# Kernel tuning notes

Measured on AMD Instinct MI355X. Metric: run time of the kernel, lower is better.

## Reference

```python
import jax, jax.numpy as jnp
import numpy as np

D_MODEL = 1024
N_HEADS = 16
HEAD_DIM = D_MODEL // N_HEADS  # 64


def setup_inputs() -> dict:
    key = jax.random.key(0)
    k1, k2, k3 = jax.random.split(key, 3)
    B, T = 2, 2048
    x = jax.random.normal(k1, (B, T, D_MODEL), dtype=jnp.float32)
    # nn.Linear(d, 3d) weight applied as x @ W (stored transposed vs torch)
    W_qkv = jax.random.normal(k2, (D_MODEL, 3 * D_MODEL), dtype=jnp.float32) / np.sqrt(D_MODEL)
    W_proj = jax.random.normal(k3, (D_MODEL, D_MODEL), dtype=jnp.float32) / np.sqrt(D_MODEL)
    return {"x": x, "W_qkv": W_qkv, "W_proj": W_proj}


def reference(x, W_qkv, W_proj):
    B, T, D = x.shape
    qkv = x @ W_qkv  # [B, T, 3D]
    qkv = qkv.reshape(B, T, 3, N_HEADS, HEAD_DIM)
    qkv = jnp.transpose(qkv, (2, 0, 3, 1, 4))  # [3, B, H, T, hd]
    q, k, v = qkv[0], qkv[1], qkv[2]
    # muP 'readout' attn_score: scale by 1/head_dim (instead of 1/sqrt(head_dim))
    attn = jnp.einsum('bhqd,bhkd->bhqk', q, k) / HEAD_DIM  # [B, H, T, T]
    attn = jax.nn.softmax(attn, axis=-1)
    out = jnp.einsum('bhqk,bhkd->bhqd', attn, v)  # [B, H, T, hd]
    out = jnp.transpose(out, (0, 2, 1, 3)).reshape(B, T, D)
    return out @ W_proj
```

## Files before the change

kernel.cpp:

```cpp
#include <hip/hip_runtime.h>
#include <hip/hip_bf16.h>
#include <hip/hip_fp16.h>
#include <stdint.h>

#define B_    2
#define T_    2048
#define DM    1024
#define NH    16
#define HD    64
#define M_    (B_ * T_)
#define N_QKV (3 * DM)

typedef __attribute__((ext_vector_type(8))) __bf16 bf16x8;
typedef __attribute__((ext_vector_type(4))) float  v4f;
typedef __attribute__((ext_vector_type(4))) _Float16 h4;
typedef __attribute__((ext_vector_type(8))) _Float16 h8;
typedef __hip_bfloat16 bf16;

__device__ __forceinline__ void gld_lds16(const void* g, void* l) {
  __builtin_amdgcn_global_load_lds(
      (const __attribute__((address_space(1))) void*)(g),
      (__attribute__((address_space(3))) void*)(l), 16, 0, 0);
}


__global__ void cast_f32_bf16(const float* __restrict__ in, bf16* __restrict__ out) {
  int i = (blockIdx.x * 256 + threadIdx.x) * 4;
  float4 v = *(const float4*)(in + i);
  union { bf16 h[4]; ushort4 u; } r;
  r.h[0] = __float2bfloat16(v.x); r.h[1] = __float2bfloat16(v.y);
  r.h[2] = __float2bfloat16(v.z); r.h[3] = __float2bfloat16(v.w);
  *(ushort4*)(out + i) = r.u;
}

__global__ void transpose_cast(const float* __restrict__ in, bf16* __restrict__ out,
                               int R, int C) {
  __shared__ float tile[32][33];
  int c0 = blockIdx.x * 32, r0 = blockIdx.y * 32;
  int tx = threadIdx.x, ty = threadIdx.y;
  #pragma unroll
  for (int i = ty; i < 32; i += 8)
    tile[i][tx] = in[(size_t)(r0 + i) * C + c0 + tx];
  __syncthreads();
  #pragma unroll
  for (int i = ty; i < 32; i += 8)
    out[(size_t)(c0 + i) * R + r0 + tx] = __float2bfloat16(tile[tx][i]);
}

__global__ __launch_bounds__(256) void transpose_v(
    const _Float16* __restrict__ in, _Float16* __restrict__ out) {
  __shared__ _Float16 tl[64][72];
  const int tid = threadIdx.x, bh = blockIdx.y, t0 = blockIdx.x * 64;
  const size_t ib = (size_t)bh * T_ * HD, ob = (size_t)bh * HD * T_;
  #pragma unroll
  for (int i = 0; i < 2; ++i) {
    int flat = (i * 256 + tid) * 8;
    int r = flat >> 6, c = flat & 63;
    *(uint4*)(&tl[r][c]) = *(const uint4*)(in + ib + (size_t)(t0 + r) * HD + c);
  }
  __syncthreads();
  int d = tid >> 2, c0 = (tid & 3) * 16;
  #pragma unroll
  for (int j = 0; j < 16; j += 8) {
    union { _Float16 h[8]; uint4 u; } pk;
    #pragma unroll
    for (int k2 = 0; k2 < 8; ++k2) pk.h[k2] = tl[c0 + j + k2][d];
    *(uint4*)(out + ob + (size_t)d * T_ + t0 + c0 + j) = pk.u;
  }
}

template <int MODE>
__global__ __launch_bounds__(256) void gemm_bt(
    const bf16* __restrict__ A, const bf16* __restrict__ BT,
    float* __restrict__ Cf, bf16* __restrict__ qb, bf16* __restrict__ kb,
    _Float16* __restrict__ vb, int M, int N, int K) {
  __shared__ bf16 As[128 * 64];
  __shared__ bf16 Bs[128 * 64];
  const int tid = threadIdx.x;
  const int l = tid & 63, w = tid >> 6;
  const int wm = w >> 1, wn = w & 1;
  const int m0 = blockIdx.y * 128, n0 = blockIdx.x * 128;
  const int fr = l & 15;
  const int lg = l >> 4;

  v4f acc[4][4] = {};

  for (int kt = 0; kt < K; kt += 64) {
    __syncthreads();
    #pragma unroll
    for (int i = 0; i < 4; ++i) {
      int p = i * 256 + tid;
      int row = p >> 3, g = (p & 7) ^ (row & 7);
      gld_lds16(A + (size_t)(m0 + row) * K + kt + g * 8, As + p * 8);
      gld_lds16(BT + (size_t)(n0 + row) * K + kt + g * 8, Bs + p * 8);
    }
    __syncthreads();
    #pragma unroll
    for (int kk = 0; kk < 64; kk += 32) {
      const int gl = (kk >> 3) + lg;
      bf16x8 af[4], bfr[4];
      #pragma unroll
      for (int i = 0; i < 4; ++i) {
        int row = wm * 64 + i * 16 + fr;
        af[i] = *(const bf16x8*)(As + row * 64 + (gl ^ (fr & 7)) * 8);
      }
      #pragma unroll
      for (int i = 0; i < 4; ++i) {
        int row = wn * 64 + i * 16 + fr;
        bfr[i] = *(const bf16x8*)(Bs + row * 64 + (gl ^ (fr & 7)) * 8);
      }
      #pragma unroll
      for (int mi = 0; mi < 4; ++mi)
        #pragma unroll
        for (int ni = 0; ni < 4; ++ni)
          acc[mi][ni] = __builtin_amdgcn_mfma_f32_16x16x32_bf16(
              af[mi], bfr[ni], acc[mi][ni], 0, 0, 0);
    }
  }

  #pragma unroll
  for (int mi = 0; mi < 4; ++mi) {
    #pragma unroll
    for (int ni = 0; ni < 4; ++ni) {
      #pragma unroll
      for (int r = 0; r < 4; ++r) {
        int gm = m0 + wm * 64 + mi * 16 + (l >> 4) * 4 + r;
        int gn = n0 + wn * 64 + ni * 16 + (l & 15);
        float v = acc[mi][ni][r];
        if constexpr (MODE == 0) {
          Cf[(size_t)gm * N + gn] = v;
        } else {
          int b = gm >> 11, t = gm & 2047;
          int s = gn >> 10, h = (gn >> 6) & 15, d = gn & 63;
          size_t bh = (size_t)(b * NH + h);
          if (s == 0)      qb[(bh * T_ + t) * HD + d] = __float2bfloat16(v);
          else if (s == 1) kb[(bh * T_ + t) * HD + d] = __float2bfloat16(v);
          else             vb[(bh * T_ + t) * HD + d] = (_Float16)v;
        }
      }
    }
  }
}

__global__ __launch_bounds__(128) void flash_attn(
    const bf16* __restrict__ Qg, const bf16* __restrict__ Kg,
    const _Float16* __restrict__ VTg, bf16* __restrict__ Og) {
  __shared__ bf16     Ks[128 * 64];
  __shared__ _Float16 Vs[64 * 128];
  __shared__ _Float16 Ps[128][40];
  const int tid = threadIdx.x, l = tid & 63, w = tid >> 6;
  const int bh = blockIdx.y, qt = blockIdx.x;
  const int fr = l & 15, fk = (l >> 4) * 8, g4 = (l >> 4) * 4, lg = l >> 4;
  const int q0 = qt * 128 + w * 64;
  const size_t base  = (size_t)bh * T_ * HD;
  const size_t baseV = (size_t)bh * HD * T_;

  bf16x8 qB[4][2];
  #pragma unroll
  for (int qf = 0; qf < 4; ++qf)
    #pragma unroll
    for (int kki = 0; kki < 2; ++kki)
      qB[qf][kki] = *(const bf16x8*)(
          Qg + base + (size_t)(q0 + qf * 16 + fr) * HD + kki * 32 + fk);

  h8 ones;
  #pragma unroll
  for (int j = 0; j < 8; ++j) ones[j] = (_Float16)1.0f;

  v4f o[4][4] = {};
  v4f lacc[4] = {};

  for (int kt = 0; kt < T_; kt += 128) {
    __syncthreads();
    #pragma unroll
    for (int i = 0; i < 8; ++i) {
      int p = i * 128 + tid;
      int krow = p >> 3, kg = (p & 7) ^ (krow & 7);
      gld_lds16(Kg + base + (size_t)(kt + krow) * HD + kg * 8, Ks + p * 8);
      int vrow = p >> 4, vg = (p & 15) ^ (vrow & 15);
      gld_lds16(VTg + baseV + (size_t)vrow * T_ + kt + vg * 8, Vs + p * 8);
    }
    __syncthreads();

    #pragma unroll
    for (int kk = 0; kk < 4; ++kk) {
      #pragma unroll
      for (int half = 0; half < 2; ++half) {
        const int kf = kk * 2 + half;
        v4f st[4] = {};
        #pragma unroll
        for (int kki = 0; kki < 2; ++kki) {
          int row = kf * 16 + fr;
          bf16x8 ak = *(const bf16x8*)(
              Ks + row * 64 + ((kki * 4 + lg) ^ (fr & 7)) * 8);
          #pragma unroll
          for (int qf = 0; qf < 4; ++qf)
            st[qf] = __builtin_amdgcn_mfma_f32_16x16x32_bf16(
                ak, qB[qf][kki], st[qf], 0, 0, 0);
        }
        #pragma unroll
        for (int qf = 0; qf < 4; ++qf) {
          h4 pv;
          #pragma unroll
          for (int r = 0; r < 4; ++r)
            pv[r] = (_Float16)__expf(st[qf][r] * 0.015625f);
          *(h4*)(&Ps[w * 64 + qf * 16 + fr][half * 16 + g4]) = pv;
        }
      }
      h8 ap[4], bv[4];
      #pragma unroll
      for (int qf = 0; qf < 4; ++qf)
        ap[qf] = *(const h8*)(&Ps[w * 64 + qf * 16 + fr][fk]);
      #pragma unroll
      for (int nf = 0; nf < 4; ++nf) {
        int row = nf * 16 + fr;
        bv[nf] = *(const h8*)(Vs + row * 128 + ((kk * 4 + lg) ^ fr) * 8);
      }
      #pragma unroll
      for (int qf = 0; qf < 4; ++qf) {
        lacc[qf] = __builtin_amdgcn_mfma_f32_16x16x32_f16(
            ap[qf], ones, lacc[qf], 0, 0, 0);
        #pragma unroll
        for (int nf = 0; nf < 4; ++nf)
          o[qf][nf] = __builtin_amdgcn_mfma_f32_16x16x32_f16(
              ap[qf], bv[nf], o[qf][nf], 0, 0, 0);
      }
    }
  }

  int b = bh >> 4, h = bh & 15;
  #pragma unroll
  for (int qf = 0; qf < 4; ++qf) {
    #pragma unroll
    for (int r = 0; r < 4; ++r) {
      float inv = 1.f / lacc[qf][r];
      int t = q0 + qf * 16 + g4 + r;
      #pragma unroll
      for (int nf = 0; nf < 4; ++nf) {
        int d = nf * 16 + fr;
        Og[((size_t)(b * T_ + t)) * DM + h * HD + d] =
            __float2bfloat16(o[qf][nf][r] * inv);
      }
    }
  }
}

extern "C" void kernel_launch(void* const* d_in, const int* in_sizes, int n_in,
                              void* d_out, int out_size, void* d_ws, size_t ws_size,
                              hipStream_t stream) {
  const float* x     = (const float*)d_in[0];
  const float* Wqkv  = (const float*)d_in[1];
  const float* Wproj = (const float*)d_in[2];
  float* out = (float*)d_out;
  char* ws = (char*)d_ws;

  bf16*     Xb     = (bf16*)(ws);
  bf16*     WqkvT  = (bf16*)(ws + (size_t)( 8u << 20));
  bf16*     WprojT = (bf16*)(ws + (size_t)(14u << 20));
  bf16*     Qb     = (bf16*)(ws + (size_t)(16u << 20));
  bf16*     Kb     = (bf16*)(ws + (size_t)(24u << 20));
  _Float16* VTh    = (_Float16*)(ws + (size_t)(32u << 20));
  _Float16* Vh     = (_Float16*)(ws + (size_t)(40u << 20));
  bf16*     Ab     = (bf16*)(ws + (size_t)(40u << 20));

  cast_f32_bf16<<<(M_ * DM) / 1024, 256, 0, stream>>>(x, Xb);
  transpose_cast<<<dim3(N_QKV / 32, DM / 32), dim3(32, 8), 0, stream>>>(Wqkv, WqkvT, DM, N_QKV);
  transpose_cast<<<dim3(DM / 32, DM / 32), dim3(32, 8), 0, stream>>>(Wproj, WprojT, DM, DM);

  gemm_bt<1><<<dim3(N_QKV / 128, M_ / 128), 256, 0, stream>>>(
      Xb, WqkvT, nullptr, Qb, Kb, Vh, M_, N_QKV, DM);

  transpose_v<<<dim3(T_ / 64, B_ * NH), 256, 0, stream>>>(Vh, VTh);

  flash_attn<<<dim3(T_ / 128, B_ * NH), 128, 0, stream>>>(Qb, Kb, VTh, Ab);

  gemm_bt<0><<<dim3(DM / 128, M_ / 128), 256, 0, stream>>>(
      Ab, WprojT, out, nullptr, nullptr, nullptr, M_, DM, DM);
}
```

Before: 215.1 us.

## Split attention keys across warps and split-K the output projection GEMM

Flash attention now runs 256 threads per block: two warp pairs each process half of every 128-key tile, and their partial O and row sums are reduced through shared memory before the write. The softmax exp is rewritten as a raw exp2 with a folded scale and packed fp16 conversion. The output projection GEMM is split along K into two halves that atomically accumulate into a zeroed output, doubling the block count. Costs are an extra memset, atomic traffic, a shared-memory reduction step, and nondeterministic float summation order.

```diff
diff --git a/kernel.cpp b/kernel.cpp
--- a/kernel.cpp
+++ b/kernel.cpp
@@ -13,9 +13,12 @@
 
 typedef __attribute__((ext_vector_type(8))) __bf16 bf16x8;
 typedef __attribute__((ext_vector_type(4))) float  v4f;
+typedef __attribute__((ext_vector_type(2))) __fp16 fp16x2;
 typedef __attribute__((ext_vector_type(4))) _Float16 h4;
 typedef __attribute__((ext_vector_type(8))) _Float16 h8;
 typedef __hip_bfloat16 bf16;
+
+#define EXP_SC 0.022542110013890053f
 
 __device__ __forceinline__ void gld_lds16(const void* g, void* l) {
   __builtin_amdgcn_global_load_lds(
@@ -85,7 +88,11 @@
 
   v4f acc[4][4] = {};
 
-  for (int kt = 0; kt < K; kt += 64) {
+  const int khalf = K >> 1;
+  const int kbeg = (MODE == 2) ? (int)blockIdx.z * khalf : 0;
+  const int kend = (MODE == 2) ? kbeg + khalf : K;
+
+  for (int kt = kbeg; kt < kend; kt += 64) {
     __syncthreads();
     #pragma unroll
     for (int i = 0; i < 4; ++i) {
@@ -129,6 +136,8 @@
         float v = acc[mi][ni][r];
         if constexpr (MODE == 0) {
           Cf[(size_t)gm * N + gn] = v;
+        } else if constexpr (MODE == 2) {
+          unsafeAtomicAdd(&Cf[(size_t)gm * N + gn], v);
         } else {
           int b = gm >> 11, t = gm & 2047;
           int s = gn >> 10, h = (gn >> 6) & 15, d = gn & 63;
@@ -142,18 +151,24 @@
   }
 }
 
-__global__ __launch_bounds__(128) void flash_attn(
+__global__ __launch_bounds__(256) void flash_attn(
     const bf16* __restrict__ Qg, const bf16* __restrict__ Kg,
     const _Float16* __restrict__ VTg, bf16* __restrict__ Og) {
-  __shared__ bf16     Ks[128 * 64];
-  __shared__ _Float16 Vs[64 * 128];
-  __shared__ _Float16 Ps[128][40];
+  __shared__ char smem[53248];
+  bf16*     Ks = (bf16*)smem;
+  _Float16* Vs = (_Float16*)(smem + 16384);
+  _Float16 (*Ps)[40] = (_Float16(*)[40])(smem + 32768);
+  float*    Obuf = (float*)smem;
+  float*    Lbuf = (float*)(smem + 34816);
+
   const int tid = threadIdx.x, l = tid & 63, w = tid >> 6;
+  const int qh = w & 1, kh = w >> 1;
+  const int fr = l & 15, fk = (l >> 4) * 8, g4 = (l >> 4) * 4, lg = l >> 4;
   const int bh = blockIdx.y, qt = blockIdx.x;
-  const int fr = l & 15, fk = (l >> 4) * 8, g4 = (l >> 4) * 4, lg = l >> 4;
-  const int q0 = qt * 128 + w * 64;
+  const int q0 = qt * 128 + qh * 64;
   const size_t base  = (size_t)bh * T_ * HD;
   const size_t baseV = (size_t)bh * HD * T_;
+  _Float16 (*Pw)[40] = Ps + w * 64;
 
   bf16x8 qB[4][2];
   #pragma unroll
@@ -173,8 +188,8 @@
   for (int kt = 0; kt < T_; kt += 128) {
     __syncthreads();
     #pragma unroll
-    for (int i = 0; i < 8; ++i) {
-      int p = i * 128 + tid;
+    for (int i = 0; i < 4; ++i) {
+      int p = i * 256 + tid;
       int krow = p >> 3, kg = (p & 7) ^ (krow & 7);
       gld_lds16(Kg + base + (size_t)(kt + krow) * HD + kg * 8, Ks + p * 8);
       int vrow = p >> 4, vg = (p & 15) ^ (vrow & 15);
@@ -183,10 +198,11 @@
     __syncthreads();
 
     #pragma unroll
-    for (int kk = 0; kk < 4; ++kk) {
-      #pragma unroll
-      for (int half = 0; half < 2; ++half) {
-        const int kf = kk * 2 + half;
+    for (int c = 0; c < 2; ++c) {
+      const int kkg = kh * 2 + c;
+      #pragma unroll
+      for (int hf = 0; hf < 2; ++hf) {
+        const int kf = kkg * 2 + hf;
         v4f st[4] = {};
         #pragma unroll
         for (int kki = 0; kki < 2; ++kki) {
@@ -200,21 +216,24 @@
         }
         #pragma unroll
         for (int qf = 0; qf < 4; ++qf) {
-          h4 pv;
-          #pragma unroll
-          for (int r = 0; r < 4; ++r)
-            pv[r] = (_Float16)__expf(st[qf][r] * 0.015625f);
-          *(h4*)(&Ps[w * 64 + qf * 16 + fr][half * 16 + g4]) = pv;
+          union { fp16x2 p2[2]; h4 p4; } u;
+          u.p2[0] = __builtin_amdgcn_cvt_pkrtz(
+              __builtin_amdgcn_exp2f(st[qf][0] * EXP_SC),
+              __builtin_amdgcn_exp2f(st[qf][1] * EXP_SC));
+          u.p2[1] = __builtin_amdgcn_cvt_pkrtz(
+              __builtin_amdgcn_exp2f(st[qf][2] * EXP_SC),
+              __builtin_amdgcn_exp2f(st[qf][3] * EXP_SC));
+          *(h4*)(&Pw[qf * 16 + fr][hf * 16 + g4]) = u.p4;
         }
       }
       h8 ap[4], bv[4];
       #pragma unroll
       for (int qf = 0; qf < 4; ++qf)
-        ap[qf] = *(const h8*)(&Ps[w * 64 + qf * 16 + fr][fk]);
+        ap[qf] = *(const h8*)(&Pw[qf * 16 + fr][fk]);
       #pragma unroll
       for (int nf = 0; nf < 4; ++nf) {
         int row = nf * 16 + fr;
-        bv[nf] = *(const h8*)(Vs + row * 128 + ((kk * 4 + lg) ^ fr) * 8);
+        bv[nf] = *(const h8*)(Vs + row * 128 + ((kkg * 4 + lg) ^ fr) * 8);
       }
       #pragma unroll
       for (int qf = 0; qf < 4; ++qf) {
@@ -228,18 +247,35 @@
     }
   }
 
-  int b = bh >> 4, h = bh & 15;
-  #pragma unroll
-  for (int qf = 0; qf < 4; ++qf) {
-    #pragma unroll
-    for (int r = 0; r < 4; ++r) {
-      float inv = 1.f / lacc[qf][r];
-      int t = q0 + qf * 16 + g4 + r;
-      #pragma unroll
-      for (int nf = 0; nf < 4; ++nf) {
-        int d = nf * 16 + fr;
-        Og[((size_t)(b * T_ + t)) * DM + h * HD + d] =
-            __float2bfloat16(o[qf][nf][r] * inv);
+  __syncthreads();
+  if (w >= 2) {
+    #pragma unroll
+    for (int qf = 0; qf < 4; ++qf)
+      #pragma unroll
+      for (int r = 0; r < 4; ++r) {
+        int row = qf * 16 + g4 + r;
+        #pragma unroll
+        for (int nf = 0; nf < 4; ++nf)
+          Obuf[(qh * 64 + row) * 68 + nf * 16 + fr] = o[qf][nf][r];
+        if (fr == 0) Lbuf[qh * 64 + row] = lacc[qf][r];
+      }
+  }
+  __syncthreads();
+  if (w < 2) {
+    int b = bh >> 4, h = bh & 15;
+    #pragma unroll
+    for (int qf = 0; qf < 4; ++qf) {
+      #pragma unroll
+      for (int r = 0; r < 4; ++r) {
+        int row = qf * 16 + g4 + r;
+        float inv = 1.f / (lacc[qf][r] + Lbuf[qh * 64 + row]);
+        int t = q0 + row;
+        #pragma unroll
+        for (int nf = 0; nf < 4; ++nf) {
+          float val = o[qf][nf][r] + Obuf[(qh * 64 + row) * 68 + nf * 16 + fr];
+          Og[((size_t)(b * T_ + t)) * DM + h * HD + nf * 16 + fr] =
+              __float2bfloat16(val * inv);
+        }
       }
     }
   }
@@ -272,8 +308,9 @@
 
   transpose_v<<<dim3(T_ / 64, B_ * NH), 256, 0, stream>>>(Vh, VTh);
 
-  flash_attn<<<dim3(T_ / 128, B_ * NH), 128, 0, stream>>>(Qb, Kb, VTh, Ab);
-
-  gemm_bt<0><<<dim3(DM / 128, M_ / 128), 256, 0, stream>>>(
+  flash_attn<<<dim3(T_ / 128, B_ * NH), 256, 0, stream>>>(Qb, Kb, VTh, Ab);
+
+  (void)hipMemsetAsync(d_out, 0, (size_t)M_ * DM * sizeof(float), stream);
+  gemm_bt<2><<<dim3(DM / 128, M_ / 128, 2), 256, 0, stream>>>(
       Ab, WprojT, out, nullptr, nullptr, nullptr, M_, DM, DM);
 }
```

Result: slower. 221.5 us (+3.0%).
